# Kernel tuning notes

Hardware: AMD Instinct MI355X
Metric: run time of the kernel (lower is better)

## Reference

```python
import jax, jax.numpy as jnp
import numpy as np

N_HEADS = 16

def setup_inputs() -> dict:
    key = jax.random.key(0)
    ks = jax.random.split(key, 5)
    D = 2048
    x = jax.random.normal(ks[0], (2, 2048, D), dtype=jnp.float32)
    scale = 1.0 / np.sqrt(D)
    Wq = jax.random.normal(ks[1], (D, D), dtype=jnp.float32) * scale
    Wk = jax.random.normal(ks[2], (D, D), dtype=jnp.float32) * scale
    Wv = jax.random.normal(ks[3], (D, D), dtype=jnp.float32) * scale
    Wo = jax.random.normal(ks[4], (D, D), dtype=jnp.float32) * scale
    return {"x": x, "Wq": Wq, "Wk": Wk, "Wv": Wv, "Wo": Wo}


def reference(x, Wq, Wk, Wv, Wo):
    # Causal multi-head attention. The original module computes it one query
    # position at a time (recompute loop) but the math is standard causal MHA:
    # query pos attends to key positions 0..pos.
    B, S, D = x.shape
    H = N_HEADS
    hd = D // H
    def split_heads(t):
        return t.reshape(B, S, H, hd).transpose(0, 2, 1, 3)  # (B,H,S,hd)
    q = split_heads(x @ Wq.T)
    k = split_heads(x @ Wk.T)
    v = split_heads(x @ Wv.T)
    scores = jnp.einsum('bhqd,bhkd->bhqk', q, k) / jnp.sqrt(jnp.asarray(hd, x.dtype))
    causal = jnp.tril(jnp.ones((S, S), dtype=bool))  # (S,S), True where allowed
    scores = jnp.where(causal[None, None], scores, jnp.asarray(-jnp.inf, scores.dtype))
    attn = jax.nn.softmax(scores, axis=-1)
    out = jnp.einsum('bhqk,bhkd->bhqd', attn, v)
    out = out.transpose(0, 2, 1, 3).reshape(B, S, D)
    return out @ Wo.T
```

## Files before the change

### kernel.cpp

```cpp
#include <hip/hip_runtime.h>
#include <stdint.h>

#define DD 2048
#define SS 2048
#define NB 2
#define NH 16
#define HDIM 128
#define MM (NB*SS)

typedef __attribute__((ext_vector_type(8))) short bf16x8;
typedef __attribute__((ext_vector_type(4))) float f32x4;
typedef __attribute__((ext_vector_type(4))) ushort u16x4;

__device__ __forceinline__ float fast_exp2(float x) {
  return __builtin_amdgcn_exp2f(x);
}

__device__ __forceinline__ ushort f2bf(float f) {
  union { float f; uint32_t u; } v; v.f = f;
  uint32_t u = v.u;
  return (ushort)((u + 0x7fffu + ((u >> 16) & 1u)) >> 16);
}

__device__ __forceinline__ void gld_lds16(const ushort* g, ushort* l) {
  __builtin_amdgcn_global_load_lds(
      (const __attribute__((address_space(1))) void*)g,
      (__attribute__((address_space(3))) void*)l, 16, 0, 0);
}

__global__ __launch_bounds__(256) void cvt_all(
    const float* __restrict__ x, const float* __restrict__ wq,
    const float* __restrict__ wk, const float* __restrict__ wv,
    const float* __restrict__ wo, ushort* __restrict__ dst)
{
  int i8 = blockIdx.x * 256 + threadIdx.x;
  const int X8 = MM * DD / 8;
  const int W8 = DD * DD / 8;
  const float* src; int off;
  if (i8 < X8)            { src = x;  off = i8; }
  else if (i8 < X8 +   W8){ src = wq; off = i8 - X8; }
  else if (i8 < X8 + 2*W8){ src = wk; off = i8 - (X8 +   W8); }
  else if (i8 < X8 + 3*W8){ src = wv; off = i8 - (X8 + 2*W8); }
  else                    { src = wo; off = i8 - (X8 + 3*W8); }
  const float4* p = (const float4*)src;
  float4 a = p[(long)off*2], b = p[(long)off*2 + 1];
  bf16x8 o;
  o[0]=(short)f2bf(a.x); o[1]=(short)f2bf(a.y); o[2]=(short)f2bf(a.z); o[3]=(short)f2bf(a.w);
  o[4]=(short)f2bf(b.x); o[5]=(short)f2bf(b.y); o[6]=(short)f2bf(b.z); o[7]=(short)f2bf(b.w);
  *(bf16x8*)(dst + (long)i8*8) = o;
}

template<int MODE>
__global__ __launch_bounds__(512, 2) void gemm8(
    const ushort* __restrict__ A, const ushort* __restrict__ Bt,
    ushort* __restrict__ Qo, ushort* __restrict__ Ko, ushort* __restrict__ Vt,
    float* __restrict__ Cf)
{
  __shared__ ushort lds[3 * 24576];
  const int NBX = (MODE == 0) ? 6 : 2;
  const int t = threadIdx.x;
  const int bid = blockIdx.x;
  const int xcd = bid & 7, local = bid >> 3;
  const int bm = local / NBX;
  const int bn = xcd * NBX + (local - bm * NBX);
  const int lane = t & 63;
  const int w = t >> 6;
  const int wr = w >> 2;
  const int wcn = w & 3;
  const int lr = lane & 15, lg = lane >> 4;

  int aoff[4], aldo[4], boff[2], bldo[2];
#pragma unroll
  for (int i = 0; i < 4; ++i) {
    int c = i*512 + t, row = c >> 3, slot = c & 7, gc = slot ^ (row & 7);
    aoff[i] = row*DD + gc*8; aldo[i] = c*8;
  }
#pragma unroll
  for (int i = 0; i < 2; ++i) {
    int c = i*512 + t, row = c >> 3, slot = c & 7, gc = slot ^ (row & 7);
    boff[i] = row*DD + gc*8; bldo[i] = 16384 + c*8;
  }
  const ushort* Ab = A  + (long)(bm*256) * DD;
  const ushort* Bb = Bt + (long)(bn*128) * DD;

#define STG_A01(KT, BUF) do { const ushort* a_ = Ab + (KT)*64;          \
    ushort* l_ = lds + (BUF)*24576;                                     \
    gld_lds16(a_ + aoff[0], l_ + aldo[0]);                              \
    gld_lds16(a_ + aoff[1], l_ + aldo[1]); } while (0)
#define STG_A23(KT, BUF) do { const ushort* a_ = Ab + (KT)*64;          \
    ushort* l_ = lds + (BUF)*24576;                                     \
    gld_lds16(a_ + aoff[2], l_ + aldo[2]);                              \
    gld_lds16(a_ + aoff[3], l_ + aldo[3]); } while (0)
#define STG_B(KT, BUF)   do { const ushort* b_ = Bb + (KT)*64;          \
    ushort* l_ = lds + (BUF)*24576;                                     \
    gld_lds16(b_ + boff[0], l_ + bldo[0]);                              \
    gld_lds16(b_ + boff[1], l_ + bldo[1]); } while (0)

#define LDA(dst, m, ks) { int row = wr*128 + (m)*16 + lr;               \
    (dst) = *(const bf16x8*)(cb + row*128 + ((((ks)*4+lg)^(row&7))*16)); }
#define LDB(dst, n, ks) { int row = wcn*32 + (n)*16 + lr;               \
    (dst) = *(const bf16x8*)(cb + 32768 + row*128 + ((((ks)*4+lg)^(row&7))*16)); }
#define MFMA8(h, av, bv) do {                                           \
    __builtin_amdgcn_s_setprio(1);                                      \
    _Pragma("unroll") for (int m = 0; m < 4; ++m)                       \
      _Pragma("unroll") for (int n = 0; n < 2; ++n)                     \
        acc[(h)*4+m][n] = __builtin_amdgcn_mfma_f32_16x16x32_bf16(      \
            av[m], bv[n], acc[(h)*4+m][n], 0, 0, 0);                    \
    __builtin_amdgcn_s_setprio(0); } while (0)
#define SB  __builtin_amdgcn_sched_barrier(0)
#define BAR __builtin_amdgcn_s_barrier()
#define LGKM0 asm volatile("s_waitcnt lgkmcnt(0)" ::: "memory")

  f32x4 acc[8][2] = {};
  const int T = DD / 64;

  STG_A01(0, 0); STG_A23(0, 0); STG_B(0, 0);
  STG_A01(1, 1); STG_A23(1, 1); STG_B(1, 1);
  asm volatile("s_waitcnt vmcnt(6)" ::: "memory");
  SB; BAR; SB;

  int bcur = 0, bs = 2;
  for (int kt = 0; kt < T; ++kt) {
    const char* cb = (const char*)lds + bcur * 49152;
    const bool st = (kt + 2 < T);
    bf16x8 a0[4], a1[4], b0[2], b1[2];
    LDA(a0[0],0,0); LDA(a0[1],1,0); LDA(a0[2],2,0); LDA(a0[3],3,0);
    LDB(b0[0],0,0); LDB(b0[1],1,0);
    if (st) STG_A01(kt+2, bs);
    SB; BAR; LGKM0; SB;
    MFMA8(0, a0, b0);
    SB; BAR; SB;
    LDA(a1[0],4,0); LDA(a1[1],5,0); LDA(a1[2],6,0); LDA(a1[3],7,0);
    if (st) STG_A23(kt+2, bs);
    SB; BAR; LGKM0; SB;
    MFMA8(1, a1, b0);
    SB; BAR; SB;
    LDA(a0[0],0,1); LDA(a0[1],1,1); LDA(a0[2],2,1); LDA(a0[3],3,1);
    LDB(b1[0],0,1); LDB(b1[1],1,1);
    if (st) STG_B(kt+2, bs);
    SB; BAR; LGKM0; SB;
    MFMA8(0, a0, b1);
    SB; BAR; SB;
    LDA(a1[0],4,1); LDA(a1[1],5,1); LDA(a1[2],6,1); LDA(a1[3],7,1);
    if (st) { asm volatile("s_waitcnt vmcnt(6)" ::: "memory"); }
    else    { asm volatile("s_waitcnt vmcnt(0)" ::: "memory"); }
    SB; BAR; LGKM0; SB;
    MFMA8(1, a1, b1);
    SB; BAR; SB;
    bcur = (bcur == 2) ? 0 : bcur + 1;
    bs   = (bs   == 2) ? 0 : bs   + 1;
  }
#undef STG_A01
#undef STG_A23
#undef STG_B
#undef LDA
#undef LDB
#undef MFMA8
#undef SB
#undef BAR
#undef LGKM0

  const int crb = bm*256 + wr*128 + lg*4;
  if (MODE == 0) {
    const int region = bn >> 4;
    const int ccb = (bn & 15)*128 + wcn*32 + lr;
    if (region < 2) {
      const float scale = (region == 0) ? (0.08838834764831845f * 1.4426950408889634f) : 1.0f;
      ushort* C = (region == 0) ? Qo : Ko;
#pragma unroll
      for (int m = 0; m < 8; ++m)
#pragma unroll
        for (int n = 0; n < 2; ++n)
#pragma unroll
          for (int j = 0; j < 4; ++j)
            C[(long)(crb + m*16 + j) * DD + (ccb + n*16)] = f2bf(acc[m][n][j] * scale);
    } else {
#pragma unroll
      for (int m = 0; m < 8; ++m) {
        int sg = crb + m*16;
        int b2 = sg >> 11, s2 = sg & 2047;
#pragma unroll
        for (int n = 0; n < 2; ++n) {
          int colv = ccb + n*16;
          int h2 = colv >> 7, d2 = colv & 127;
          u16x4 pk;
          pk[0] = f2bf(acc[m][n][0]); pk[1] = f2bf(acc[m][n][1]);
          pk[2] = f2bf(acc[m][n][2]); pk[3] = f2bf(acc[m][n][3]);
          *(u16x4*)(Vt + ((long)((b2*NH + h2)*HDIM + d2)) * SS + s2) = pk;
        }
      }
    }
  } else {
    const int ccb = bn*128 + wcn*32 + lr;
#pragma unroll
    for (int m = 0; m < 8; ++m)
#pragma unroll
      for (int n = 0; n < 2; ++n)
#pragma unroll
        for (int j = 0; j < 4; ++j)
          Cf[(long)(crb + m*16 + j) * DD + (ccb + n*16)] = acc[m][n][j];
  }
}

__global__ __launch_bounds__(512, 4) void attn_fwd(
    const ushort* __restrict__ Qb, const ushort* __restrict__ Kb,
    const ushort* __restrict__ Vtg, ushort* __restrict__ Ob)
{
  __shared__ ushort Ks[64*128];
  __shared__ ushort Vs[128*64];
  __shared__ ushort Ps[8*16*72];

  const int bid = blockIdx.x;
  const int qt = 15 - (bid >> 5);
  const int bh = bid & 31;
  const int b = bh >> 4, h = bh & 15;
  const int t = threadIdx.x;
  const int lane = t & 63;
  const int wq = t >> 6;
  const int lr = lane & 15, lg = lane >> 4;

  const int qbase = qt * 128;
  const long rowQ = (long)(b * SS + qbase + wq * 16);

  bf16x8 qf[4];
#pragma unroll
  for (int c = 0; c < 4; ++c)
    qf[c] = *(const bf16x8*)(Qb + (rowQ + lr) * DD + h*HDIM + c*32 + lg*8);

  f32x4 accO[8] = {};
  float mrow[4], lrow[4];
#pragma unroll
  for (int j = 0; j < 4; ++j) { mrow[j] = -1e30f; lrow[j] = 0.f; }

  const ushort* Kgb = Kb + (long)(b * SS) * DD + h * HDIM;
  const int kr0 = t >> 4, kr1 = 32 + (t >> 4), kci = t & 15;
  const ushort* gk0 = Kgb + (long)kr0 * DD + (kci ^ (kr0 & 7)) * 8;
  const ushort* gk1 = Kgb + (long)kr1 * DD + (kci ^ (kr1 & 7)) * 8;
  ushort* lk0 = Ks + t*8;
  ushort* lk1 = Ks + 4096 + t*8;

  const ushort* Vgb = Vtg + (long)(bh * HDIM) * SS;
  const int vd0 = t >> 3, vd1 = 64 + (t >> 3), vci = t & 7;
  const ushort* gv0 = Vgb + (long)vd0 * SS + (vci ^ (vd0 & 7)) * 8;
  const ushort* gv1 = Vgb + (long)vd1 * SS + (vci ^ (vd1 & 7)) * 8;
  ushort* lv0 = Vs + t*8;
  ushort* lv1 = Vs + 4096 + t*8;

  const int ktmax = 2*qt + 1;
  const int qminw = qbase + wq*16;
  const int qmaxw = qminw + 15;
  ushort* myP = Ps + wq * (16*72);

  for (int kt = 0; kt <= ktmax; ++kt) {
    const int k0 = kt * 64;
    gld_lds16(gk0, lk0); gld_lds16(gk1, lk1);
    gld_lds16(gv0, lv0); gld_lds16(gv1, lv1);
    gk0 += (long)64 * DD; gk1 += (long)64 * DD;
    gv0 += 64; gv1 += 64;
    __syncthreads();

    if (k0 <= qmaxw) {
      f32x4 sc[4] = {};
#pragma unroll
      for (int n = 0; n < 4; ++n) {
        int r = n*16 + lr;
        int swz = (r & 7) << 4;
#pragma unroll
        for (int c = 0; c < 4; ++c) {
          bf16x8 kf = *(const bf16x8*)((const char*)Ks + ((r*256 + c*64 + lg*16) ^ swz));
          sc[n] = __builtin_amdgcn_mfma_f32_16x16x32_bf16(qf[c], kf, sc[n], 0,0,0);
        }
      }
      if (k0 + 63 > qminw) {
#pragma unroll
        for (int n = 0; n < 4; ++n)
#pragma unroll
          for (int j = 0; j < 4; ++j) {
            int kpos = k0 + n*16 + lr;
            int qpos = qminw + lg*4 + j;
            if (kpos > qpos) sc[n][j] = -1e30f;
          }
      }
      float al[4];
#pragma unroll
      for (int j = 0; j < 4; ++j) {
        float tm = fmaxf(fmaxf(sc[0][j], sc[1][j]), fmaxf(sc[2][j], sc[3][j]));
#pragma unroll
        for (int off = 1; off < 16; off <<= 1) tm = fmaxf(tm, __shfl_xor(tm, off));
        float mn = fmaxf(mrow[j], tm);
        float a = fast_exp2(mrow[j] - mn);
        mrow[j] = mn;
        float ts = 0.f;
#pragma unroll
        for (int n = 0; n < 4; ++n) {
          float p = fast_exp2(sc[n][j] - mn);
          sc[n][j] = p; ts += p;
        }
#pragma unroll
        for (int off = 1; off < 16; off <<= 1) ts += __shfl_xor(ts, off);
        lrow[j] = lrow[j] * a + ts;
        al[j] = a;
      }
#pragma unroll
      for (int dg = 0; dg < 8; ++dg) {
        f32x4 v = accO[dg];
        v[0] *= al[0]; v[1] *= al[1]; v[2] *= al[2]; v[3] *= al[3];
        accO[dg] = v;
      }
#pragma unroll
      for (int n = 0; n < 4; ++n)
#pragma unroll
        for (int j = 0; j < 4; ++j)
          myP[(lg*4 + j)*72 + n*16 + lr] = f2bf(sc[n][j]);
      bf16x8 pa0 = *(const bf16x8*)(myP + lr*72 + lg*8);
      bf16x8 pa1 = *(const bf16x8*)(myP + lr*72 + 32 + lg*8);
#pragma unroll
      for (int dg = 0; dg < 8; ++dg) {
        int d = dg*16 + lr;
        int vswz = (d & 7) << 4;
        bf16x8 v0 = *(const bf16x8*)((const char*)Vs + ((d*128 + lg*16) ^ vswz));
        bf16x8 v1 = *(const bf16x8*)((const char*)Vs + ((d*128 + 64 + lg*16) ^ vswz));
        accO[dg] = __builtin_amdgcn_mfma_f32_16x16x32_bf16(pa0, v0, accO[dg], 0,0,0);
        accO[dg] = __builtin_amdgcn_mfma_f32_16x16x32_bf16(pa1, v1, accO[dg], 0,0,0);
      }
    }
    __syncthreads();
  }

  float inv[4];
#pragma unroll
  for (int j = 0; j < 4; ++j) inv[j] = 1.0f / lrow[j];
  ushort* Og = Ob + rowQ * DD + h * HDIM;
#pragma unroll
  for (int dg = 0; dg < 8; ++dg)
#pragma unroll
    for (int j = 0; j < 4; ++j)
      Og[(long)(lg*4 + j) * DD + dg*16 + lr] = f2bf(accO[dg][j] * inv[j]);
}

extern "C" void kernel_launch(void* const* d_in, const int* in_sizes, int n_in,
                              void* d_out, int out_size, void* d_ws, size_t ws_size,
                              hipStream_t stream) {
  const float* x  = (const float*)d_in[0];
  const float* Wq = (const float*)d_in[1];
  const float* Wk = (const float*)d_in[2];
  const float* Wv = (const float*)d_in[3];
  const float* Wo = (const float*)d_in[4];

  ushort* ws  = (ushort*)d_ws;
  ushort* xb  = ws;
  ushort* wqb = ws  + (long)MM*DD;
  ushort* wkb = wqb + (long)DD*DD;
  ushort* wvb = wkb + (long)DD*DD;
  ushort* wob = wvb + (long)DD*DD;
  ushort* Qb  = wob + (long)DD*DD;
  ushort* Kb  = Qb  + (long)MM*DD;
  ushort* Vtg = Kb  + (long)MM*DD;
  (void)wkb; (void)wvb;

  const int CVT_BLOCKS = (MM*DD + 4*DD*DD) / 8 / 256;
  cvt_all<<<CVT_BLOCKS, 256, 0, stream>>>(x, Wq, Wk, Wv, Wo, ws);

  gemm8<0><<<768, 512, 0, stream>>>(xb, wqb, Qb, Kb, Vtg, nullptr);

  attn_fwd<<<512, 512, 0, stream>>>(Qb, Kb, Vtg, xb);

  gemm8<1><<<256, 512, 0, stream>>>(xb, wob, nullptr, nullptr, nullptr,
                                    (float*)d_out);
}
```

Baseline: 280.5 us.

## Enlarge GEMM tiles to 256x256 with double-buffered LDS staging

The projection GEMMs move from 256x128 output tiles with triple-buffered LDS to 256x256 tiles with double buffering. Each wave now computes a 128x64 sub-tile, and the launch grids are halved accordingly. The larger tile raises arithmetic intensity per LDS and global byte. The cost is 128KB of LDS per block, which allows only one block per CU. It also leaves 384 and 128 blocks to cover 256 CUs, and prefetch is cut to one tile ahead with a full vmcnt(0) wait each iteration.

```diff
diff --git a/kernel.cpp b/kernel.cpp
--- a/kernel.cpp
+++ b/kernel.cpp
@@ -51,154 +51,155 @@
 }
 
 template<int MODE>
-__global__ __launch_bounds__(512, 2) void gemm8(
+__global__ __launch_bounds__(512, 2) void gemm256(
     const ushort* __restrict__ A, const ushort* __restrict__ Bt,
     ushort* __restrict__ Qo, ushort* __restrict__ Ko, ushort* __restrict__ Vt,
     float* __restrict__ Cf)
 {
-  __shared__ ushort lds[3 * 24576];
-  const int NBX = (MODE == 0) ? 6 : 2;
+  __shared__ ushort lds[65536];
   const int t = threadIdx.x;
   const int bid = blockIdx.x;
   const int xcd = bid & 7, local = bid >> 3;
+  const int NBX = (MODE == 0) ? 3 : 1;
   const int bm = local / NBX;
   const int bn = xcd * NBX + (local - bm * NBX);
-  const int lane = t & 63;
-  const int w = t >> 6;
+  const int lane = t & 63, w = t >> 6;
   const int wr = w >> 2;
   const int wcn = w & 3;
   const int lr = lane & 15, lg = lane >> 4;
 
-  int aoff[4], aldo[4], boff[2], bldo[2];
+  int aoff[4], aldo[4];
 #pragma unroll
   for (int i = 0; i < 4; ++i) {
     int c = i*512 + t, row = c >> 3, slot = c & 7, gc = slot ^ (row & 7);
     aoff[i] = row*DD + gc*8; aldo[i] = c*8;
   }
-#pragma unroll
-  for (int i = 0; i < 2; ++i) {
-    int c = i*512 + t, row = c >> 3, slot = c & 7, gc = slot ^ (row & 7);
-    boff[i] = row*DD + gc*8; bldo[i] = 16384 + c*8;
-  }
   const ushort* Ab = A  + (long)(bm*256) * DD;
-  const ushort* Bb = Bt + (long)(bn*128) * DD;
-
-#define STG_A01(KT, BUF) do { const ushort* a_ = Ab + (KT)*64;          \
-    ushort* l_ = lds + (BUF)*24576;                                     \
-    gld_lds16(a_ + aoff[0], l_ + aldo[0]);                              \
-    gld_lds16(a_ + aoff[1], l_ + aldo[1]); } while (0)
-#define STG_A23(KT, BUF) do { const ushort* a_ = Ab + (KT)*64;          \
-    ushort* l_ = lds + (BUF)*24576;                                     \
-    gld_lds16(a_ + aoff[2], l_ + aldo[2]);                              \
-    gld_lds16(a_ + aoff[3], l_ + aldo[3]); } while (0)
-#define STG_B(KT, BUF)   do { const ushort* b_ = Bb + (KT)*64;          \
-    ushort* l_ = lds + (BUF)*24576;                                     \
-    gld_lds16(b_ + boff[0], l_ + bldo[0]);                              \
-    gld_lds16(b_ + boff[1], l_ + bldo[1]); } while (0)
-
-#define LDA(dst, m, ks) { int row = wr*128 + (m)*16 + lr;               \
-    (dst) = *(const bf16x8*)(cb + row*128 + ((((ks)*4+lg)^(row&7))*16)); }
-#define LDB(dst, n, ks) { int row = wcn*32 + (n)*16 + lr;               \
-    (dst) = *(const bf16x8*)(cb + 32768 + row*128 + ((((ks)*4+lg)^(row&7))*16)); }
-#define MFMA8(h, av, bv) do {                                           \
-    __builtin_amdgcn_s_setprio(1);                                      \
-    _Pragma("unroll") for (int m = 0; m < 4; ++m)                       \
-      _Pragma("unroll") for (int n = 0; n < 2; ++n)                     \
-        acc[(h)*4+m][n] = __builtin_amdgcn_mfma_f32_16x16x32_bf16(      \
-            av[m], bv[n], acc[(h)*4+m][n], 0, 0, 0);                    \
+  const ushort* Bb = Bt + (long)(bn*256) * DD;
+
+#define STG_A(P, KT, D) do { const ushort* g_ = Ab + (KT)*64;              \
+    ushort* l_ = lds + (D)*16384;                                          \
+    gld_lds16(g_ + aoff[2*(P)],   l_ + aldo[2*(P)]);                       \
+    gld_lds16(g_ + aoff[2*(P)+1], l_ + aldo[2*(P)+1]); } while (0)
+#define STG_B(P, KT, D) do { const ushort* g_ = Bb + (KT)*64;              \
+    ushort* l_ = lds + 32768 + (D)*16384;                                  \
+    gld_lds16(g_ + aoff[2*(P)],   l_ + aldo[2*(P)]);                       \
+    gld_lds16(g_ + aoff[2*(P)+1], l_ + aldo[2*(P)+1]); } while (0)
+#define LDA(dst, MH, m, ks) { int r_ = wr*128 + (MH)*64 + (m)*16 + lr;     \
+    (dst) = *(const bf16x8*)(ab + r_*128 + ((((ks)*4+lg)^(r_&7))*16)); }
+#define LDB(dst, NH_, n, ks) { int r_ = wcn*64 + (NH_)*32 + (n)*16 + lr;   \
+    (dst) = *(const bf16x8*)(bb + r_*128 + ((((ks)*4+lg)^(r_&7))*16)); }
+#define MFMA16(AV, BV, MB, NBASE) do {                                     \
+    __builtin_amdgcn_s_setprio(1);                                         \
+    _Pragma("unroll") for (int ks = 0; ks < 2; ++ks)                       \
+    _Pragma("unroll") for (int m = 0; m < 4; ++m)                          \
+    _Pragma("unroll") for (int n = 0; n < 2; ++n)                          \
+      acc[(MB)+m][(NBASE)+n] = __builtin_amdgcn_mfma_f32_16x16x32_bf16(    \
+          AV[m][ks], BV[n][ks], acc[(MB)+m][(NBASE)+n], 0, 0, 0);          \
     __builtin_amdgcn_s_setprio(0); } while (0)
 #define SB  __builtin_amdgcn_sched_barrier(0)
 #define BAR __builtin_amdgcn_s_barrier()
 #define LGKM0 asm volatile("s_waitcnt lgkmcnt(0)" ::: "memory")
 
-  f32x4 acc[8][2] = {};
+  f32x4 acc[8][4] = {};
   const int T = DD / 64;
 
-  STG_A01(0, 0); STG_A23(0, 0); STG_B(0, 0);
-  STG_A01(1, 1); STG_A23(1, 1); STG_B(1, 1);
-  asm volatile("s_waitcnt vmcnt(6)" ::: "memory");
+  STG_A(0, 0, 0); STG_A(1, 0, 0); STG_B(0, 0, 0); STG_B(1, 0, 0);
+  asm volatile("s_waitcnt vmcnt(0)" ::: "memory");
   SB; BAR; SB;
 
-  int bcur = 0, bs = 2;
   for (int kt = 0; kt < T; ++kt) {
-    const char* cb = (const char*)lds + bcur * 49152;
-    const bool st = (kt + 2 < T);
-    bf16x8 a0[4], a1[4], b0[2], b1[2];
-    LDA(a0[0],0,0); LDA(a0[1],1,0); LDA(a0[2],2,0); LDA(a0[3],3,0);
-    LDB(b0[0],0,0); LDB(b0[1],1,0);
-    if (st) STG_A01(kt+2, bs);
+    const char* ab = (const char*)lds + (kt & 1) * 32768;
+    const char* bb = (const char*)lds + 65536 + (kt & 1) * 32768;
+    const int wd = (kt + 1) & 1;
+    const bool st = (kt + 1 < T);
+    bf16x8 af0[4][2], af1[4][2], bf[2][2];
+    LDA(af0[0][0],0,0,0); LDA(af0[1][0],0,1,0); LDA(af0[2][0],0,2,0); LDA(af0[3][0],0,3,0);
+    LDA(af0[0][1],0,0,1); LDA(af0[1][1],0,1,1); LDA(af0[2][1],0,2,1); LDA(af0[3][1],0,3,1);
+    LDB(bf[0][0],0,0,0);  LDB(bf[1][0],0,1,0);
+    LDB(bf[0][1],0,0,1);  LDB(bf[1][1],0,1,1);
+    if (st) { STG_A(0, kt+1, wd); STG_A(1, kt+1, wd); }
     SB; BAR; LGKM0; SB;
-    MFMA8(0, a0, b0);
-    SB; BAR; SB;
-    LDA(a1[0],4,0); LDA(a1[1],5,0); LDA(a1[2],6,0); LDA(a1[3],7,0);
-    if (st) STG_A23(kt+2, bs);
+    MFMA16(af0, bf, 0, 0);
+    SB; BAR; SB;
+    LDA(af1[0][0],1,0,0); LDA(af1[1][0],1,1,0); LDA(af1[2][0],1,2,0); LDA(af1[3][0],1,3,0);
+    LDA(af1[0][1],1,0,1); LDA(af1[1][1],1,1,1); LDA(af1[2][1],1,2,1); LDA(af1[3][1],1,3,1);
+    if (st) { STG_B(0, kt+1, wd); STG_B(1, kt+1, wd); }
     SB; BAR; LGKM0; SB;
-    MFMA8(1, a1, b0);
-    SB; BAR; SB;
-    LDA(a0[0],0,1); LDA(a0[1],1,1); LDA(a0[2],2,1); LDA(a0[3],3,1);
-    LDB(b1[0],0,1); LDB(b1[1],1,1);
-    if (st) STG_B(kt+2, bs);
+    MFMA16(af1, bf, 4, 0);
+    SB; BAR; SB;
+    LDB(bf[0][0],1,0,0);  LDB(bf[1][0],1,1,0);
+    LDB(bf[0][1],1,0,1);  LDB(bf[1][1],1,1,1);
     SB; BAR; LGKM0; SB;
-    MFMA8(0, a0, b1);
-    SB; BAR; SB;
-    LDA(a1[0],4,1); LDA(a1[1],5,1); LDA(a1[2],6,1); LDA(a1[3],7,1);
-    if (st) { asm volatile("s_waitcnt vmcnt(6)" ::: "memory"); }
-    else    { asm volatile("s_waitcnt vmcnt(0)" ::: "memory"); }
-    SB; BAR; LGKM0; SB;
-    MFMA8(1, a1, b1);
-    SB; BAR; SB;
-    bcur = (bcur == 2) ? 0 : bcur + 1;
-    bs   = (bs   == 2) ? 0 : bs   + 1;
+    MFMA16(af1, bf, 4, 2);
+    SB; BAR; SB;
+    if (st) { asm volatile("s_waitcnt vmcnt(0)" ::: "memory"); }
+    SB; BAR; SB;
+    MFMA16(af0, bf, 0, 2);
+    SB; BAR; SB;
   }
-#undef STG_A01
-#undef STG_A23
+#undef STG_A
 #undef STG_B
 #undef LDA
 #undef LDB
-#undef MFMA8
+#undef MFMA16
 #undef SB
 #undef BAR
 #undef LGKM0
 
   const int crb = bm*256 + wr*128 + lg*4;
   if (MODE == 0) {
-    const int region = bn >> 4;
-    const int ccb = (bn & 15)*128 + wcn*32 + lr;
+    const int region = bn >> 3;
+    const int ccb = (bn & 7)*256 + wcn*64 + lr;
     if (region < 2) {
       const float scale = (region == 0) ? (0.08838834764831845f * 1.4426950408889634f) : 1.0f;
       ushort* C = (region == 0) ? Qo : Ko;
 #pragma unroll
-      for (int m = 0; m < 8; ++m)
-#pragma unroll
-        for (int n = 0; n < 2; ++n)
-#pragma unroll
-          for (int j = 0; j < 4; ++j)
-            C[(long)(crb + m*16 + j) * DD + (ccb + n*16)] = f2bf(acc[m][n][j] * scale);
+      for (int mh = 0; mh < 2; ++mh)
+#pragma unroll
+        for (int m = 0; m < 4; ++m)
+#pragma unroll
+          for (int nh = 0; nh < 2; ++nh)
+#pragma unroll
+            for (int n = 0; n < 2; ++n)
+#pragma unroll
+              for (int j = 0; j < 4; ++j)
+                C[(long)(crb + mh*64 + m*16 + j) * DD + (ccb + nh*32 + n*16)] =
+                    f2bf(acc[mh*4+m][nh*2+n][j] * scale);
     } else {
 #pragma unroll
-      for (int m = 0; m < 8; ++m) {
-        int sg = crb + m*16;
-        int b2 = sg >> 11, s2 = sg & 2047;
-#pragma unroll
-        for (int n = 0; n < 2; ++n) {
-          int colv = ccb + n*16;
-          int h2 = colv >> 7, d2 = colv & 127;
-          u16x4 pk;
-          pk[0] = f2bf(acc[m][n][0]); pk[1] = f2bf(acc[m][n][1]);
-          pk[2] = f2bf(acc[m][n][2]); pk[3] = f2bf(acc[m][n][3]);
-          *(u16x4*)(Vt + ((long)((b2*NH + h2)*HDIM + d2)) * SS + s2) = pk;
+      for (int mh = 0; mh < 2; ++mh)
+#pragma unroll
+        for (int m = 0; m < 4; ++m) {
+          int sg = crb + mh*64 + m*16;
+          int b2 = sg >> 11, s2 = sg & 2047;
+#pragma unroll
+          for (int nh = 0; nh < 2; ++nh)
+#pragma unroll
+            for (int n = 0; n < 2; ++n) {
+              int colv = ccb + nh*32 + n*16;
+              int h2 = colv >> 7, d2 = colv & 127;
+              u16x4 pk;
+              pk[0] = f2bf(acc[mh*4+m][nh*2+n][0]); pk[1] = f2bf(acc[mh*4+m][nh*2+n][1]);
+              pk[2] = f2bf(acc[mh*4+m][nh*2+n][2]); pk[3] = f2bf(acc[mh*4+m][nh*2+n][3]);
+              *(u16x4*)(Vt + ((long)((b2*NH + h2)*HDIM + d2)) * SS + s2) = pk;
+            }
         }
-      }
     }
   } else {
-    const int ccb = bn*128 + wcn*32 + lr;
-#pragma unroll
-    for (int m = 0; m < 8; ++m)
-#pragma unroll
-      for (int n = 0; n < 2; ++n)
-#pragma unroll
-        for (int j = 0; j < 4; ++j)
-          Cf[(long)(crb + m*16 + j) * DD + (ccb + n*16)] = acc[m][n][j];
+    const int ccb = bn*256 + wcn*64 + lr;
+#pragma unroll
+    for (int mh = 0; mh < 2; ++mh)
+#pragma unroll
+      for (int m = 0; m < 4; ++m)
+#pragma unroll
+        for (int nh = 0; nh < 2; ++nh)
+#pragma unroll
+          for (int n = 0; n < 2; ++n)
+#pragma unroll
+            for (int j = 0; j < 4; ++j)
+              Cf[(long)(crb + mh*64 + m*16 + j) * DD + (ccb + nh*32 + n*16)] =
+                  acc[mh*4+m][nh*2+n][j];
   }
 }
 
@@ -361,10 +362,10 @@
   const int CVT_BLOCKS = (MM*DD + 4*DD*DD) / 8 / 256;
   cvt_all<<<CVT_BLOCKS, 256, 0, stream>>>(x, Wq, Wk, Wv, Wo, ws);
 
-  gemm8<0><<<768, 512, 0, stream>>>(xb, wqb, Qb, Kb, Vtg, nullptr);
+  gemm256<0><<<384, 512, 0, stream>>>(xb, wqb, Qb, Kb, Vtg, nullptr);
 
   attn_fwd<<<512, 512, 0, stream>>>(Qb, Kb, Vtg, xb);
 
-  gemm8<1><<<256, 512, 0, stream>>>(xb, wob, nullptr, nullptr, nullptr,
-                                    (float*)d_out);
-}
+  gemm256<1><<<128, 512, 0, stream>>>(xb, wob, nullptr, nullptr, nullptr,
+                                      (float*)d_out);
+}
```

Result: slower. 302.4 us (+7.8%).

## Restructure GEMM to 4-wave blocks with 32-wide K tiles and 128x64 warp tiles

Applied to the files above, without the earlier changes.

The projection GEMMs drop from 8 waves to 4 waves per 256x128 block, so each wave now computes a 128x64 subtile with 32 accumulators instead of 16. The K step shrinks from 64 to 32, with a new packed LDS layout that stores two rows per 128-byte line under an XOR swizzle, which halves the per-stage LDS footprint. The aim is more register-level reuse of A and B fragments per LDS read, at the cost of higher register pressure, twice as many loop iterations and barriers, and fewer waves to hide latency.

```diff
diff --git a/kernel.cpp b/kernel.cpp
--- a/kernel.cpp
+++ b/kernel.cpp
@@ -51,111 +51,106 @@
 }
 
 template<int MODE>
-__global__ __launch_bounds__(512, 2) void gemm8(
+__global__ __launch_bounds__(256, 2) void gemm_tri(
     const ushort* __restrict__ A, const ushort* __restrict__ Bt,
     ushort* __restrict__ Qo, ushort* __restrict__ Ko, ushort* __restrict__ Vt,
     float* __restrict__ Cf)
 {
-  __shared__ ushort lds[3 * 24576];
-  const int NBX = (MODE == 0) ? 6 : 2;
+  __shared__ ushort lds[3 * 12288];
   const int t = threadIdx.x;
   const int bid = blockIdx.x;
   const int xcd = bid & 7, local = bid >> 3;
+  const int NBX = (MODE == 0) ? 6 : 2;
   const int bm = local / NBX;
   const int bn = xcd * NBX + (local - bm * NBX);
-  const int lane = t & 63;
-  const int w = t >> 6;
-  const int wr = w >> 2;
-  const int wcn = w & 3;
+  const int lane = t & 63, w = t >> 6;
+  const int wr = w >> 1, wcn = w & 1;
   const int lr = lane & 15, lg = lane >> 4;
 
-  int aoff[4], aldo[4], boff[2], bldo[2];
+  int aoff[4], boff[2];
 #pragma unroll
   for (int i = 0; i < 4; ++i) {
-    int c = i*512 + t, row = c >> 3, slot = c & 7, gc = slot ^ (row & 7);
-    aoff[i] = row*DD + gc*8; aldo[i] = c*8;
+    int p = i*256 + t, ln = p >> 3, sr = (p & 7) ^ (ln & 7);
+    aoff[i] = (2*ln + (sr >> 2)) * DD + (sr & 3) * 8;
   }
 #pragma unroll
   for (int i = 0; i < 2; ++i) {
-    int c = i*512 + t, row = c >> 3, slot = c & 7, gc = slot ^ (row & 7);
-    boff[i] = row*DD + gc*8; bldo[i] = 16384 + c*8;
+    int p = i*256 + t, ln = p >> 3, sr = (p & 7) ^ (ln & 7);
+    boff[i] = (2*ln + (sr >> 2)) * DD + (sr & 3) * 8;
   }
   const ushort* Ab = A  + (long)(bm*256) * DD;
   const ushort* Bb = Bt + (long)(bn*128) * DD;
 
-#define STG_A01(KT, BUF) do { const ushort* a_ = Ab + (KT)*64;          \
-    ushort* l_ = lds + (BUF)*24576;                                     \
-    gld_lds16(a_ + aoff[0], l_ + aldo[0]);                              \
-    gld_lds16(a_ + aoff[1], l_ + aldo[1]); } while (0)
-#define STG_A23(KT, BUF) do { const ushort* a_ = Ab + (KT)*64;          \
-    ushort* l_ = lds + (BUF)*24576;                                     \
-    gld_lds16(a_ + aoff[2], l_ + aldo[2]);                              \
-    gld_lds16(a_ + aoff[3], l_ + aldo[3]); } while (0)
-#define STG_B(KT, BUF)   do { const ushort* b_ = Bb + (KT)*64;          \
-    ushort* l_ = lds + (BUF)*24576;                                     \
-    gld_lds16(b_ + boff[0], l_ + bldo[0]);                              \
-    gld_lds16(b_ + boff[1], l_ + bldo[1]); } while (0)
-
-#define LDA(dst, m, ks) { int row = wr*128 + (m)*16 + lr;               \
-    (dst) = *(const bf16x8*)(cb + row*128 + ((((ks)*4+lg)^(row&7))*16)); }
-#define LDB(dst, n, ks) { int row = wcn*32 + (n)*16 + lr;               \
-    (dst) = *(const bf16x8*)(cb + 32768 + row*128 + ((((ks)*4+lg)^(row&7))*16)); }
-#define MFMA8(h, av, bv) do {                                           \
-    __builtin_amdgcn_s_setprio(1);                                      \
-    _Pragma("unroll") for (int m = 0; m < 4; ++m)                       \
-      _Pragma("unroll") for (int n = 0; n < 2; ++n)                     \
-        acc[(h)*4+m][n] = __builtin_amdgcn_mfma_f32_16x16x32_bf16(      \
-            av[m], bv[n], acc[(h)*4+m][n], 0, 0, 0);                    \
+#define STG_A01(KT, BUF) do { const ushort* g_ = Ab + (KT)*32;             \
+    ushort* l_ = lds + (BUF)*12288;                                        \
+    gld_lds16(g_ + aoff[0], l_ + t*8);                                     \
+    gld_lds16(g_ + aoff[1], l_ + (256 + t)*8); } while (0)
+#define STG_A23(KT, BUF) do { const ushort* g_ = Ab + (KT)*32;             \
+    ushort* l_ = lds + (BUF)*12288;                                        \
+    gld_lds16(g_ + aoff[2], l_ + (512 + t)*8);                             \
+    gld_lds16(g_ + aoff[3], l_ + (768 + t)*8); } while (0)
+#define STG_B(KT, BUF)   do { const ushort* g_ = Bb + (KT)*32;             \
+    ushort* l_ = lds + (BUF)*12288 + 8192;                                 \
+    gld_lds16(g_ + boff[0], l_ + t*8);                                     \
+    gld_lds16(g_ + boff[1], l_ + (256 + t)*8); } while (0)
+#define LDA(dst, m) { int r_ = wr*128 + (m)*16 + lr; int ln_ = r_ >> 1;    \
+    int sl_ = (lg + ((r_ & 1) << 2)) ^ (ln_ & 7);                          \
+    (dst) = *(const bf16x8*)(cb + ln_*128 + sl_*16); }
+#define LDB(dst, n) { int r_ = wcn*64 + (n)*16 + lr; int ln_ = r_ >> 1;    \
+    int sl_ = (lg + ((r_ & 1) << 2)) ^ (ln_ & 7);                          \
+    (dst) = *(const bf16x8*)(cb + 16384 + ln_*128 + sl_*16); }
+#define MFMA42(AV, BV, MB, NB_) do {                                       \
+    __builtin_amdgcn_s_setprio(1);                                         \
+    _Pragma("unroll") for (int m = 0; m < 4; ++m)                          \
+    _Pragma("unroll") for (int n = 0; n < 2; ++n)                          \
+      acc[(MB)+m][(NB_)+n] = __builtin_amdgcn_mfma_f32_16x16x32_bf16(      \
+          AV[m], BV[n], acc[(MB)+m][(NB_)+n], 0, 0, 0);                    \
     __builtin_amdgcn_s_setprio(0); } while (0)
 #define SB  __builtin_amdgcn_sched_barrier(0)
 #define BAR __builtin_amdgcn_s_barrier()
 #define LGKM0 asm volatile("s_waitcnt lgkmcnt(0)" ::: "memory")
 
-  f32x4 acc[8][2] = {};
-  const int T = DD / 64;
+  f32x4 acc[8][4] = {};
+  const int T = DD / 32;
 
   STG_A01(0, 0); STG_A23(0, 0); STG_B(0, 0);
   STG_A01(1, 1); STG_A23(1, 1); STG_B(1, 1);
   asm volatile("s_waitcnt vmcnt(6)" ::: "memory");
   SB; BAR; SB;
 
-  int bcur = 0, bs = 2;
   for (int kt = 0; kt < T; ++kt) {
-    const char* cb = (const char*)lds + bcur * 49152;
+    const char* cb = (const char*)lds + (kt % 3) * 24576;
+    const int bs = (kt + 2) % 3;
     const bool st = (kt + 2 < T);
-    bf16x8 a0[4], a1[4], b0[2], b1[2];
-    LDA(a0[0],0,0); LDA(a0[1],1,0); LDA(a0[2],2,0); LDA(a0[3],3,0);
-    LDB(b0[0],0,0); LDB(b0[1],1,0);
+    bf16x8 a03[4], a47[4], b01[2], b23[2];
+    LDA(a03[0],0); LDA(a03[1],1); LDA(a03[2],2); LDA(a03[3],3);
+    LDB(b01[0],0); LDB(b01[1],1);
     if (st) STG_A01(kt+2, bs);
     SB; BAR; LGKM0; SB;
-    MFMA8(0, a0, b0);
-    SB; BAR; SB;
-    LDA(a1[0],4,0); LDA(a1[1],5,0); LDA(a1[2],6,0); LDA(a1[3],7,0);
+    MFMA42(a03, b01, 0, 0);
+    SB; BAR; SB;
+    LDA(a47[0],4); LDA(a47[1],5); LDA(a47[2],6); LDA(a47[3],7);
     if (st) STG_A23(kt+2, bs);
     SB; BAR; LGKM0; SB;
-    MFMA8(1, a1, b0);
-    SB; BAR; SB;
-    LDA(a0[0],0,1); LDA(a0[1],1,1); LDA(a0[2],2,1); LDA(a0[3],3,1);
-    LDB(b1[0],0,1); LDB(b1[1],1,1);
+    MFMA42(a47, b01, 4, 0);
+    SB; BAR; SB;
+    LDB(b23[0],2); LDB(b23[1],3);
     if (st) STG_B(kt+2, bs);
     SB; BAR; LGKM0; SB;
-    MFMA8(0, a0, b1);
-    SB; BAR; SB;
-    LDA(a1[0],4,1); LDA(a1[1],5,1); LDA(a1[2],6,1); LDA(a1[3],7,1);
-    if (st) { asm volatile("s_waitcnt vmcnt(6)" ::: "memory"); }
-    else    { asm volatile("s_waitcnt vmcnt(0)" ::: "memory"); }
-    SB; BAR; LGKM0; SB;
-    MFMA8(1, a1, b1);
-    SB; BAR; SB;
-    bcur = (bcur == 2) ? 0 : bcur + 1;
-    bs   = (bs   == 2) ? 0 : bs   + 1;
+    MFMA42(a03, b23, 0, 2);
+    SB; BAR; SB;
+    if (st)              { asm volatile("s_waitcnt vmcnt(6)" ::: "memory"); }
+    else if (kt + 1 < T) { asm volatile("s_waitcnt vmcnt(0)" ::: "memory"); }
+    SB; BAR; SB;
+    MFMA42(a47, b23, 4, 2);
+    SB; BAR; SB;
   }
 #undef STG_A01
 #undef STG_A23
 #undef STG_B
 #undef LDA
 #undef LDB
-#undef MFMA8
+#undef MFMA42
 #undef SB
 #undef BAR
 #undef LGKM0
@@ -163,14 +158,14 @@
   const int crb = bm*256 + wr*128 + lg*4;
   if (MODE == 0) {
     const int region = bn >> 4;
-    const int ccb = (bn & 15)*128 + wcn*32 + lr;
+    const int ccb = (bn & 15)*128 + wcn*64 + lr;
     if (region < 2) {
       const float scale = (region == 0) ? (0.08838834764831845f * 1.4426950408889634f) : 1.0f;
       ushort* C = (region == 0) ? Qo : Ko;
 #pragma unroll
       for (int m = 0; m < 8; ++m)
 #pragma unroll
-        for (int n = 0; n < 2; ++n)
+        for (int n = 0; n < 4; ++n)
 #pragma unroll
           for (int j = 0; j < 4; ++j)
             C[(long)(crb + m*16 + j) * DD + (ccb + n*16)] = f2bf(acc[m][n][j] * scale);
@@ -180,7 +175,7 @@
         int sg = crb + m*16;
         int b2 = sg >> 11, s2 = sg & 2047;
 #pragma unroll
-        for (int n = 0; n < 2; ++n) {
+        for (int n = 0; n < 4; ++n) {
           int colv = ccb + n*16;
           int h2 = colv >> 7, d2 = colv & 127;
           u16x4 pk;
@@ -191,11 +186,11 @@
       }
     }
   } else {
-    const int ccb = bn*128 + wcn*32 + lr;
+    const int ccb = bn*128 + wcn*64 + lr;
 #pragma unroll
     for (int m = 0; m < 8; ++m)
 #pragma unroll
-      for (int n = 0; n < 2; ++n)
+      for (int n = 0; n < 4; ++n)
 #pragma unroll
         for (int j = 0; j < 4; ++j)
           Cf[(long)(crb + m*16 + j) * DD + (ccb + n*16)] = acc[m][n][j];
@@ -361,10 +356,10 @@
   const int CVT_BLOCKS = (MM*DD + 4*DD*DD) / 8 / 256;
   cvt_all<<<CVT_BLOCKS, 256, 0, stream>>>(x, Wq, Wk, Wv, Wo, ws);
 
-  gemm8<0><<<768, 512, 0, stream>>>(xb, wqb, Qb, Kb, Vtg, nullptr);
+  gemm_tri<0><<<768, 256, 0, stream>>>(xb, wqb, Qb, Kb, Vtg, nullptr);
 
   attn_fwd<<<512, 512, 0, stream>>>(Qb, Kb, Vtg, xb);
 
-  gemm8<1><<<256, 512, 0, stream>>>(xb, wob, nullptr, nullptr, nullptr,
-                                    (float*)d_out);
-}
+  gemm_tri<1><<<256, 256, 0, stream>>>(xb, wob, nullptr, nullptr, nullptr,
+                                       (float*)d_out);
+}
```

After: 274.8 us. -2.0%, faster.
